# Kernel optimization log

Measured on AMD Instinct MI355X. Metric: run time of the kernel, lower is better.

Reference implementation:

```python
import jax, jax.numpy as jnp
import numpy as np

NEG = -1.0e9

def setup_inputs() -> dict:
    key = jax.random.key(0)
    k1, k2 = jax.random.split(key)
    B, S, D = 4, 4096, 256
    encodings = jax.random.normal(k1, (B, S, D), dtype=jnp.float32)
    # nn.Linear weight [out, in]; Linear applies x @ W.T
    W = jax.random.normal(k2, (D, D), dtype=jnp.float32) * (1.0 / np.sqrt(D))
    return {"encodings": encodings, "W": W}

def reference(encodings, W):
    B, S, D = encodings.shape
    enc_mult_W = jnp.einsum('bsd,ed->bse', encodings, W)          # Linear, no bias
    sims = jnp.einsum('bqd,bkd->bqk', encodings, enc_mult_W)       # E @ (EW^T)^T
    scaled = sims / jnp.asarray(np.sqrt(D), dtype=sims.dtype)
    # causal mask: positions k > q masked out (top-left softmax == 1)
    mask = jnp.triu(jnp.ones((S, S), dtype=bool), k=1)
    scaled = jnp.where(mask[None, :, :], jnp.asarray(NEG, scaled.dtype), scaled)
    attn = jax.nn.softmax(scaled, axis=-1)
    return jnp.einsum('bqk,bkd->bqd', attn, encodings)
```

## Files before the change

### kernel.cpp

```cpp
#include <hip/hip_runtime.h>
#include <hip/hip_bf16.h>
#include <cstdint>
#include <cstddef>

typedef __attribute__((ext_vector_type(4))) float f32x4;
typedef __attribute__((ext_vector_type(8))) short s16x8;
typedef __attribute__((ext_vector_type(4))) unsigned int u32x4;

#define SDIM 4096
#define DDIM 256

#define GLOAD_LDS16(g, s)                                                      \
  __builtin_amdgcn_global_load_lds(                                            \
      (const __attribute__((address_space(1))) void*)(g),                      \
      (__attribute__((address_space(3))) void*)(s), 16, 0, 0)

__device__ __forceinline__ unsigned short cvt_bf16(float f) {
  union { float f; unsigned int u; } v;
  v.f = f;
  unsigned int u = v.u;
  unsigned int r = (u + 0x7FFFu + ((u >> 16) & 1u)) >> 16;
  return (unsigned short)r;
}

__device__ __forceinline__ float bf2f(unsigned short s) {
  union { unsigned int u; float f; } v;
  v.u = ((unsigned int)s) << 16;
  return v.f;
}

__global__ __launch_bounds__(256) void k_prep(const float* __restrict__ E,
                                              const float* __restrict__ W,
                                              unsigned short* __restrict__ Wb,
                                              unsigned short* __restrict__ Vt) {
  __shared__ float tile[64][65];
  const int bid = blockIdx.x;
  const int tid = threadIdx.x;
  if (bid >= 1024) {
    int i = ((bid - 1024) * 256 + tid) * 8;
    f32x4 a = *(const f32x4*)(W + i);
    f32x4 b = *(const f32x4*)(W + i + 4);
    s16x8 o;
#pragma unroll
    for (int j = 0; j < 4; ++j) {
      o[j] = (short)cvt_bf16(a[j]);
      o[4 + j] = (short)cvt_bf16(b[j]);
    }
    *(s16x8*)(Wb + i) = o;
    return;
  }
  const int b = bid >> 8;
  const int d0 = ((bid >> 6) & 3) * 64, s0 = (bid & 63) * 64;
  const int tx = tid & 63, ty = tid >> 6;
#pragma unroll
  for (int i = 0; i < 16; ++i) {
    int sr = i * 4 + ty;
    tile[sr][tx] = E[((size_t)(b * SDIM) + s0 + sr) * DDIM + d0 + tx];
  }
  __syncthreads();
#pragma unroll
  for (int i = 0; i < 16; ++i) {
    int dr = i * 4 + ty;
    Vt[((size_t)(b * DDIM) + d0 + dr) * SDIM + s0 + tx] = cvt_bf16(tile[tx][dr]);
  }
}

__global__ __launch_bounds__(256) void k_proj(const float* __restrict__ E,
                                              const unsigned short* __restrict__ Wb,
                                              unsigned short* __restrict__ Kp) {
  const int tid = threadIdx.x;
  const int w = tid >> 6, l = tid & 63, lhi = l >> 4, llo = l & 15;
  const int m0 = blockIdx.x * 64 + w * 16;
  f32x4 acc[16];
#pragma unroll
  for (int n = 0; n < 16; ++n) acc[n] = (f32x4){0.f, 0.f, 0.f, 0.f};
  const float* arow = E + (size_t)(m0 + llo) * DDIM;
#pragma unroll
  for (int kd = 0; kd < 8; ++kd) {
    const int dbase = kd * 32 + lhi * 8;
    f32x4 a0 = *(const f32x4*)(arow + dbase);
    f32x4 a1 = *(const f32x4*)(arow + dbase + 4);
    s16x8 af;
#pragma unroll
    for (int j = 0; j < 4; ++j) {
      af[j] = (short)cvt_bf16(a0[j]);
      af[4 + j] = (short)cvt_bf16(a1[j]);
    }
#pragma unroll
    for (int n = 0; n < 16; ++n) {
      s16x8 bf = *(const s16x8*)(Wb + (n * 16 + llo) * DDIM + dbase);
      acc[n] = __builtin_amdgcn_mfma_f32_16x16x32_bf16(af, bf, acc[n], 0, 0, 0);
    }
  }
  const float sc = 1.4426950408889634f / 16.0f;
#pragma unroll
  for (int n = 0; n < 16; ++n) {
#pragma unroll
    for (int r = 0; r < 4; ++r) {
      Kp[(size_t)(m0 + lhi * 4 + r) * DDIM + n * 16 + llo] = cvt_bf16(acc[n][r] * sc);
    }
  }
}

__global__ __launch_bounds__(256, 2) void k_attn(const float* __restrict__ E,
                                                 const unsigned short* __restrict__ Kp,
                                                 const unsigned short* __restrict__ Vt,
                                                 unsigned short* __restrict__ Po,
                                                 float* __restrict__ Lp, int nch) {
  __shared__ u32x4 smem4[4736];
  char* smem = (char*)smem4;
  const int tid = threadIdx.x;
  const int l = tid & 63, w = tid >> 6, lhi = l >> 4, llo = l & 15;
  const int u = blockIdx.x % (4 * nch);
  const int p = blockIdx.x / (4 * nch);
  const int b = u & 3, ch = u >> 2;
  const int chb = ch * 4 + b;

  const int trow = tid >> 5;
  const int kcolb = ((tid & 31) << 4) ^ ((trow & 7) << 4);
  const char* KpB = (const char*)Kp + (size_t)b * SDIM * 512;
  const char* VtB = (const char*)Vt + (size_t)b * DDIM * (SDIM * 2);
  const char* vsb = VtB + (size_t)(tid >> 2) * 8192 + (size_t)((tid & 3) * 8) * 2;
  char* sPw = smem + 65536 + w * 2560;

  for (int c2 = 0; c2 < 2; ++c2) {
    const int qt = c2 ? (31 - p) : p;
    const int q0 = qt * 128;
    const int ntile = 4 * (qt + 1);
    if (ntile <= ch) continue;
    const int nst = (ntile - ch + nch - 1) / nch;
    const int wq0 = q0 + w * 32;

    if (c2) __syncthreads();

    s16x8 qf[2][8];
#pragma unroll
    for (int s = 0; s < 2; ++s) {
      const float* Eq = E + ((size_t)(b * SDIM) + wq0 + s * 16 + llo) * DDIM;
#pragma unroll
      for (int kd = 0; kd < 8; ++kd) {
        f32x4 a0 = *(const f32x4*)(Eq + kd * 32 + lhi * 8);
        f32x4 a1 = *(const f32x4*)(Eq + kd * 32 + lhi * 8 + 4);
#pragma unroll
        for (int j = 0; j < 4; ++j) {
          qf[s][kd][j] = (short)cvt_bf16(a0[j]);
          qf[s][kd][4 + j] = (short)cvt_bf16(a1[j]);
        }
      }
    }

    f32x4 oT[2][16];
#pragma unroll
    for (int s = 0; s < 2; ++s)
#pragma unroll
      for (int n = 0; n < 16; ++n) oT[s][n] = (f32x4){0.f, 0.f, 0.f, 0.f};
    float lsum[2] = {0.f, 0.f};

    auto stage = [&](int t) {
      const int kv0 = (ch + nch * t) * 32;
      char* kdst = smem + ((t & 1) * 16384);
      char* vdst = smem + 32768 + ((t & 1) * 16384);
      const char* ks = KpB + (size_t)(kv0 + trow) * 512 + kcolb;
      const char* vs = vsb + (size_t)kv0 * 2;
#pragma unroll
      for (int i = 0; i < 4; ++i)
        GLOAD_LDS16(ks + (size_t)i * 4096, kdst + i * 4096 + tid * 16);
#pragma unroll
      for (int i = 0; i < 4; ++i)
        GLOAD_LDS16(vs + (size_t)i * (64 * 8192), vdst + i * 4096 + tid * 16);
    };

    stage(0);

    for (int t = 0; t < nst; ++t) {
      const int kv0 = (ch + nch * t) * 32;
      const char* kb_ = smem + ((t & 1) * 16384);
      const char* vb_ = smem + 32768 + ((t & 1) * 16384);

      __syncthreads();
      if (t + 1 < nst) stage(t + 1);

#pragma unroll
      for (int kb = 0; kb < 2; ++kb) {
        f32x4 sa0 = (f32x4){0.f, 0.f, 0.f, 0.f};
        f32x4 sa1 = (f32x4){0.f, 0.f, 0.f, 0.f};
        const char* krow = kb_ + (kb * 16 + llo) * 512;
        __builtin_amdgcn_s_setprio(1);
#pragma unroll
        for (int kd = 0; kd < 8; ++kd) {
          s16x8 kf = *(const s16x8*)(krow + ((kd * 64 + lhi * 16) ^ ((llo & 7) << 4)));
          sa0 = __builtin_amdgcn_mfma_f32_16x16x32_bf16(kf, qf[0][kd], sa0, 0, 0, 0);
          sa1 = __builtin_amdgcn_mfma_f32_16x16x32_bf16(kf, qf[1][kd], sa1, 0, 0, 0);
        }
        __builtin_amdgcn_s_setprio(0);
        const int kvr = kv0 + kb * 16 + lhi * 4;
#pragma unroll
        for (int s = 0; s < 2; ++s) {
          const f32x4 sa = s ? sa1 : sa0;
          const int qi = wq0 + s * 16 + llo;
          float pv[4];
#pragma unroll
          for (int rr = 0; rr < 4; ++rr) {
            float v = exp2f(sa[rr] - 32.0f);
            pv[rr] = (kvr + rr > qi) ? 0.0f : v;
          }
          lsum[s] += (pv[0] + pv[1]) + (pv[2] + pv[3]);
          unsigned int w0 = __builtin_amdgcn_perm(__float_as_uint(pv[1]),
                                                  __float_as_uint(pv[0]), 0x07060302u);
          unsigned int w1 = __builtin_amdgcn_perm(__float_as_uint(pv[3]),
                                                  __float_as_uint(pv[2]), 0x07060302u);
          *(uint2*)(sPw + (s * 16 + llo) * 80 + kb * 32 + lhi * 8) = make_uint2(w0, w1);
        }
      }

      s16x8 pb0 = *(const s16x8*)(sPw + llo * 80 + lhi * 16);
      s16x8 pb1 = *(const s16x8*)(sPw + (16 + llo) * 80 + lhi * 16);
      __builtin_amdgcn_s_setprio(1);
#pragma unroll
      for (int n = 0; n < 16; ++n) {
        s16x8 vf = *(const s16x8*)(vb_ + (n * 16 + llo) * 64 + lhi * 16);
        oT[0][n] = __builtin_amdgcn_mfma_f32_16x16x32_bf16(vf, pb0, oT[0][n], 0, 0, 0);
        oT[1][n] = __builtin_amdgcn_mfma_f32_16x16x32_bf16(vf, pb1, oT[1][n], 0, 0, 0);
      }
      __builtin_amdgcn_s_setprio(0);
    }

#pragma unroll
    for (int s = 0; s < 2; ++s) {
      lsum[s] += __shfl_xor(lsum[s], 16);
      lsum[s] += __shfl_xor(lsum[s], 32);
    }
#pragma unroll
    for (int s = 0; s < 2; ++s) {
      const int q = wq0 + s * 16 + llo;
      unsigned short* PoW = Po + ((size_t)chb * SDIM + q) * DDIM;
#pragma unroll
      for (int n = 0; n < 16; ++n) {
        unsigned int w0 = (unsigned int)cvt_bf16(oT[s][n][0]) |
                          ((unsigned int)cvt_bf16(oT[s][n][1]) << 16);
        unsigned int w1 = (unsigned int)cvt_bf16(oT[s][n][2]) |
                          ((unsigned int)cvt_bf16(oT[s][n][3]) << 16);
        *(uint2*)(PoW + n * 16 + lhi * 4) = make_uint2(w0, w1);
      }
      if (lhi == 0) Lp[(size_t)chb * SDIM + q] = lsum[s];
    }
  }
}

__global__ __launch_bounds__(256) void k_merge(const unsigned short* __restrict__ Po,
                                               const float* __restrict__ Lp,
                                               float* __restrict__ out, int nch) {
  const size_t e = ((size_t)blockIdx.x * 256 + threadIdx.x) * 8;
  const size_t f = e >> 8;
  const int s = (int)(f & 4095);
  const int cnt = min(nch, 4 * (s >> 7) + 4);
  float lt = 0.f;
  for (int c = 0; c < cnt; ++c) lt += Lp[(size_t)c * 16384 + f];
  const float inv = 1.0f / lt;
  float acc[8] = {0.f, 0.f, 0.f, 0.f, 0.f, 0.f, 0.f, 0.f};
  for (int c = 0; c < cnt; ++c) {
    s16x8 a = *(const s16x8*)(Po + (size_t)c * 4194304 + e);
#pragma unroll
    for (int j = 0; j < 8; ++j) acc[j] += bf2f((unsigned short)a[j]);
  }
  f32x4 o0, o1;
#pragma unroll
  for (int j = 0; j < 4; ++j) {
    o0[j] = acc[j] * inv;
    o1[j] = acc[4 + j] * inv;
  }
  *(f32x4*)(out + e) = o0;
  *(f32x4*)(out + e + 4) = o1;
}

extern "C" void kernel_launch(void* const* d_in, const int* in_sizes, int n_in,
                              void* d_out, int out_size, void* d_ws, size_t ws_size,
                              hipStream_t stream) {
  (void)in_sizes; (void)n_in; (void)out_size;
  const float* E = (const float*)d_in[0];
  const float* W = (const float*)d_in[1];
  float* out = (float*)d_out;
  char* ws = (char*)d_ws;

  const size_t base = 16777216ull;
  auto need = [&](int c) {
    return base + (size_t)c * 8388608ull + (size_t)c * 65536ull + 262144ull;
  };
  int nch = 2;
  if (ws_size >= need(8)) nch = 8;
  else if (ws_size >= need(4)) nch = 4;

  unsigned short* Kp = (unsigned short*)(ws);
  unsigned short* Vt = (unsigned short*)(ws + 8388608);
  unsigned short* Po = (unsigned short*)(ws + base);
  size_t lp_off = base + (size_t)nch * 8388608ull;
  float* Lp = (float*)(ws + lp_off);
  unsigned short* Wb = (unsigned short*)(ws + lp_off + (size_t)nch * 65536ull);

  k_prep<<<dim3(1056), dim3(256), 0, stream>>>(E, W, Wb, Vt);
  k_proj<<<dim3(256), dim3(256), 0, stream>>>(E, Wb, Kp);
  k_attn<<<dim3(16 * 4 * nch), dim3(256), 0, stream>>>(E, Kp, Vt, Po, Lp, nch);
  k_merge<<<dim3(2048), dim3(256), 0, stream>>>(Po, Lp, out, nch);
}
```

Before: 128.5 us.

## Fuse V transpose into projection, split paired q-tiles into separate blocks, nontemporal stores

The V transpose-and-convert moves out of the prep kernel and into the projection kernel, reusing the bf16 E tile already staged in LDS, so E is read once fewer. The attention kernel no longer pairs q-tile p with 31-p inside one block. Each block now handles a single q-tile, with twice as many blocks launched and the heaviest tiles scheduled first. This gives up the built-in load balancing of pairing in exchange for finer-grained scheduling. Partial outputs and the Lp sums use nontemporal stores and loads to reduce cache pollution.

```diff
diff --git a/kernel.cpp b/kernel.cpp
--- a/kernel.cpp
+++ b/kernel.cpp
@@ -29,48 +29,29 @@
   return v.f;
 }
 
-__global__ __launch_bounds__(256) void k_prep(const float* __restrict__ E,
-                                              const float* __restrict__ W,
-                                              unsigned short* __restrict__ Wb,
-                                              unsigned short* __restrict__ Vt) {
-  __shared__ float tile[64][65];
-  const int bid = blockIdx.x;
-  const int tid = threadIdx.x;
-  if (bid >= 1024) {
-    int i = ((bid - 1024) * 256 + tid) * 8;
-    f32x4 a = *(const f32x4*)(W + i);
-    f32x4 b = *(const f32x4*)(W + i + 4);
-    s16x8 o;
-#pragma unroll
-    for (int j = 0; j < 4; ++j) {
-      o[j] = (short)cvt_bf16(a[j]);
-      o[4 + j] = (short)cvt_bf16(b[j]);
-    }
-    *(s16x8*)(Wb + i) = o;
-    return;
-  }
-  const int b = bid >> 8;
-  const int d0 = ((bid >> 6) & 3) * 64, s0 = (bid & 63) * 64;
-  const int tx = tid & 63, ty = tid >> 6;
-#pragma unroll
-  for (int i = 0; i < 16; ++i) {
-    int sr = i * 4 + ty;
-    tile[sr][tx] = E[((size_t)(b * SDIM) + s0 + sr) * DDIM + d0 + tx];
-  }
-  __syncthreads();
-#pragma unroll
-  for (int i = 0; i < 16; ++i) {
-    int dr = i * 4 + ty;
-    Vt[((size_t)(b * DDIM) + d0 + dr) * SDIM + s0 + tx] = cvt_bf16(tile[tx][dr]);
-  }
-}
-
-__global__ __launch_bounds__(256) void k_proj(const float* __restrict__ E,
-                                              const unsigned short* __restrict__ Wb,
-                                              unsigned short* __restrict__ Kp) {
+__global__ __launch_bounds__(256) void k_convw(const float* __restrict__ W,
+                                               unsigned short* __restrict__ Wb) {
+  int i = (blockIdx.x * 256 + threadIdx.x) * 8;
+  f32x4 a = *(const f32x4*)(W + i);
+  f32x4 b = *(const f32x4*)(W + i + 4);
+  s16x8 o;
+#pragma unroll
+  for (int j = 0; j < 4; ++j) {
+    o[j] = (short)cvt_bf16(a[j]);
+    o[4 + j] = (short)cvt_bf16(b[j]);
+  }
+  *(s16x8*)(Wb + i) = o;
+}
+
+__global__ __launch_bounds__(256) void k_projv(const float* __restrict__ E,
+                                               const unsigned short* __restrict__ Wb,
+                                               unsigned short* __restrict__ Kp,
+                                               unsigned short* __restrict__ Vt) {
+  __shared__ unsigned short tile[64][264];
   const int tid = threadIdx.x;
   const int w = tid >> 6, l = tid & 63, lhi = l >> 4, llo = l & 15;
-  const int m0 = blockIdx.x * 64 + w * 16;
+  const int m0g = blockIdx.x * 64;
+  const int m0 = m0g + w * 16;
   f32x4 acc[16];
 #pragma unroll
   for (int n = 0; n < 16; ++n) acc[n] = (f32x4){0.f, 0.f, 0.f, 0.f};
@@ -86,10 +67,24 @@
       af[j] = (short)cvt_bf16(a0[j]);
       af[4 + j] = (short)cvt_bf16(a1[j]);
     }
+    *(s16x8*)(&tile[w * 16 + llo][dbase]) = af;
 #pragma unroll
     for (int n = 0; n < 16; ++n) {
       s16x8 bf = *(const s16x8*)(Wb + (n * 16 + llo) * DDIM + dbase);
       acc[n] = __builtin_amdgcn_mfma_f32_16x16x32_bf16(af, bf, acc[n], 0, 0, 0);
+    }
+  }
+  __syncthreads();
+  {
+    const int d = tid;
+    const int b = m0g >> 12, s0 = m0g & 4095;
+    unsigned short* vo = Vt + ((size_t)(b * DDIM) + d) * SDIM + s0;
+#pragma unroll
+    for (int g = 0; g < 8; ++g) {
+      s16x8 pk;
+#pragma unroll
+      for (int j = 0; j < 8; ++j) pk[j] = (short)tile[g * 8 + j][d];
+      *(s16x8*)(vo + g * 8) = pk;
     }
   }
   const float sc = 1.4426950408889634f / 16.0f;
@@ -112,138 +107,135 @@
   const int tid = threadIdx.x;
   const int l = tid & 63, w = tid >> 6, lhi = l >> 4, llo = l & 15;
   const int u = blockIdx.x % (4 * nch);
-  const int p = blockIdx.x / (4 * nch);
+  const int t_ = blockIdx.x / (4 * nch);
+  const int qt = 31 - t_;
   const int b = u & 3, ch = u >> 2;
+  const int q0 = qt * 128;
   const int chb = ch * 4 + b;
+  const int ntile = 4 * (qt + 1);
+  if (ntile <= ch) return;
+  const int nst = (ntile - ch + nch - 1) / nch;
+  const int wq0 = q0 + w * 32;
+
+  s16x8 qf[2][8];
+#pragma unroll
+  for (int s = 0; s < 2; ++s) {
+    const float* Eq = E + ((size_t)(b * SDIM) + wq0 + s * 16 + llo) * DDIM;
+#pragma unroll
+    for (int kd = 0; kd < 8; ++kd) {
+      f32x4 a0 = *(const f32x4*)(Eq + kd * 32 + lhi * 8);
+      f32x4 a1 = *(const f32x4*)(Eq + kd * 32 + lhi * 8 + 4);
+#pragma unroll
+      for (int j = 0; j < 4; ++j) {
+        qf[s][kd][j] = (short)cvt_bf16(a0[j]);
+        qf[s][kd][4 + j] = (short)cvt_bf16(a1[j]);
+      }
+    }
+  }
+
+  f32x4 oT[2][16];
+#pragma unroll
+  for (int s = 0; s < 2; ++s)
+#pragma unroll
+    for (int n = 0; n < 16; ++n) oT[s][n] = (f32x4){0.f, 0.f, 0.f, 0.f};
+  float lsum[2] = {0.f, 0.f};
 
   const int trow = tid >> 5;
   const int kcolb = ((tid & 31) << 4) ^ ((trow & 7) << 4);
   const char* KpB = (const char*)Kp + (size_t)b * SDIM * 512;
   const char* VtB = (const char*)Vt + (size_t)b * DDIM * (SDIM * 2);
   const char* vsb = VtB + (size_t)(tid >> 2) * 8192 + (size_t)((tid & 3) * 8) * 2;
+
+  auto stage = [&](int t) {
+    const int kv0 = (ch + nch * t) * 32;
+    char* kdst = smem + ((t & 1) * 16384);
+    char* vdst = smem + 32768 + ((t & 1) * 16384);
+    const char* ks = KpB + (size_t)(kv0 + trow) * 512 + kcolb;
+    const char* vs = vsb + (size_t)kv0 * 2;
+#pragma unroll
+    for (int i = 0; i < 4; ++i)
+      GLOAD_LDS16(ks + (size_t)i * 4096, kdst + i * 4096 + tid * 16);
+#pragma unroll
+    for (int i = 0; i < 4; ++i)
+      GLOAD_LDS16(vs + (size_t)i * (64 * 8192), vdst + i * 4096 + tid * 16);
+  };
+
+  stage(0);
   char* sPw = smem + 65536 + w * 2560;
 
-  for (int c2 = 0; c2 < 2; ++c2) {
-    const int qt = c2 ? (31 - p) : p;
-    const int q0 = qt * 128;
-    const int ntile = 4 * (qt + 1);
-    if (ntile <= ch) continue;
-    const int nst = (ntile - ch + nch - 1) / nch;
-    const int wq0 = q0 + w * 32;
-
-    if (c2) __syncthreads();
-
-    s16x8 qf[2][8];
-#pragma unroll
-    for (int s = 0; s < 2; ++s) {
-      const float* Eq = E + ((size_t)(b * SDIM) + wq0 + s * 16 + llo) * DDIM;
+  for (int t = 0; t < nst; ++t) {
+    const int kv0 = (ch + nch * t) * 32;
+    const char* kb_ = smem + ((t & 1) * 16384);
+    const char* vb_ = smem + 32768 + ((t & 1) * 16384);
+
+    __syncthreads();
+    if (t + 1 < nst) stage(t + 1);
+
+#pragma unroll
+    for (int kb = 0; kb < 2; ++kb) {
+      f32x4 sa0 = (f32x4){0.f, 0.f, 0.f, 0.f};
+      f32x4 sa1 = (f32x4){0.f, 0.f, 0.f, 0.f};
+      const char* krow = kb_ + (kb * 16 + llo) * 512;
+      __builtin_amdgcn_s_setprio(1);
 #pragma unroll
       for (int kd = 0; kd < 8; ++kd) {
-        f32x4 a0 = *(const f32x4*)(Eq + kd * 32 + lhi * 8);
-        f32x4 a1 = *(const f32x4*)(Eq + kd * 32 + lhi * 8 + 4);
-#pragma unroll
-        for (int j = 0; j < 4; ++j) {
-          qf[s][kd][j] = (short)cvt_bf16(a0[j]);
-          qf[s][kd][4 + j] = (short)cvt_bf16(a1[j]);
-        }
-      }
-    }
-
-    f32x4 oT[2][16];
-#pragma unroll
-    for (int s = 0; s < 2; ++s)
-#pragma unroll
-      for (int n = 0; n < 16; ++n) oT[s][n] = (f32x4){0.f, 0.f, 0.f, 0.f};
-    float lsum[2] = {0.f, 0.f};
-
-    auto stage = [&](int t) {
-      const int kv0 = (ch + nch * t) * 32;
-      char* kdst = smem + ((t & 1) * 16384);
-      char* vdst = smem + 32768 + ((t & 1) * 16384);
-      const char* ks = KpB + (size_t)(kv0 + trow) * 512 + kcolb;
-      const char* vs = vsb + (size_t)kv0 * 2;
-#pragma unroll
-      for (int i = 0; i < 4; ++i)
-        GLOAD_LDS16(ks + (size_t)i * 4096, kdst + i * 4096 + tid * 16);
-#pragma unroll
-      for (int i = 0; i < 4; ++i)
-        GLOAD_LDS16(vs + (size_t)i * (64 * 8192), vdst + i * 4096 + tid * 16);
-    };
-
-    stage(0);
-
-    for (int t = 0; t < nst; ++t) {
-      const int kv0 = (ch + nch * t) * 32;
-      const char* kb_ = smem + ((t & 1) * 16384);
-      const char* vb_ = smem + 32768 + ((t & 1) * 16384);
-
-      __syncthreads();
-      if (t + 1 < nst) stage(t + 1);
-
-#pragma unroll
-      for (int kb = 0; kb < 2; ++kb) {
-        f32x4 sa0 = (f32x4){0.f, 0.f, 0.f, 0.f};
-        f32x4 sa1 = (f32x4){0.f, 0.f, 0.f, 0.f};
-        const char* krow = kb_ + (kb * 16 + llo) * 512;
-        __builtin_amdgcn_s_setprio(1);
-#pragma unroll
-        for (int kd = 0; kd < 8; ++kd) {
-          s16x8 kf = *(const s16x8*)(krow + ((kd * 64 + lhi * 16) ^ ((llo & 7) << 4)));
-          sa0 = __builtin_amdgcn_mfma_f32_16x16x32_bf16(kf, qf[0][kd], sa0, 0, 0, 0);
-          sa1 = __builtin_amdgcn_mfma_f32_16x16x32_bf16(kf, qf[1][kd], sa1, 0, 0, 0);
-        }
-        __builtin_amdgcn_s_setprio(0);
-        const int kvr = kv0 + kb * 16 + lhi * 4;
-#pragma unroll
-        for (int s = 0; s < 2; ++s) {
-          const f32x4 sa = s ? sa1 : sa0;
-          const int qi = wq0 + s * 16 + llo;
-          float pv[4];
-#pragma unroll
-          for (int rr = 0; rr < 4; ++rr) {
-            float v = exp2f(sa[rr] - 32.0f);
-            pv[rr] = (kvr + rr > qi) ? 0.0f : v;
-          }
-          lsum[s] += (pv[0] + pv[1]) + (pv[2] + pv[3]);
-          unsigned int w0 = __builtin_amdgcn_perm(__float_as_uint(pv[1]),
-                                                  __float_as_uint(pv[0]), 0x07060302u);
-          unsigned int w1 = __builtin_amdgcn_perm(__float_as_uint(pv[3]),
-                                                  __float_as_uint(pv[2]), 0x07060302u);
-          *(uint2*)(sPw + (s * 16 + llo) * 80 + kb * 32 + lhi * 8) = make_uint2(w0, w1);
-        }
-      }
-
-      s16x8 pb0 = *(const s16x8*)(sPw + llo * 80 + lhi * 16);
-      s16x8 pb1 = *(const s16x8*)(sPw + (16 + llo) * 80 + lhi * 16);
-      __builtin_amdgcn_s_setprio(1);
-#pragma unroll
-      for (int n = 0; n < 16; ++n) {
-        s16x8 vf = *(const s16x8*)(vb_ + (n * 16 + llo) * 64 + lhi * 16);
-        oT[0][n] = __builtin_amdgcn_mfma_f32_16x16x32_bf16(vf, pb0, oT[0][n], 0, 0, 0);
-        oT[1][n] = __builtin_amdgcn_mfma_f32_16x16x32_bf16(vf, pb1, oT[1][n], 0, 0, 0);
+        s16x8 kf = *(const s16x8*)(krow + ((kd * 64 + lhi * 16) ^ ((llo & 7) << 4)));
+        sa0 = __builtin_amdgcn_mfma_f32_16x16x32_bf16(kf, qf[0][kd], sa0, 0, 0, 0);
+        sa1 = __builtin_amdgcn_mfma_f32_16x16x32_bf16(kf, qf[1][kd], sa1, 0, 0, 0);
       }
       __builtin_amdgcn_s_setprio(0);
-    }
-
-#pragma unroll
-    for (int s = 0; s < 2; ++s) {
-      lsum[s] += __shfl_xor(lsum[s], 16);
-      lsum[s] += __shfl_xor(lsum[s], 32);
-    }
-#pragma unroll
-    for (int s = 0; s < 2; ++s) {
-      const int q = wq0 + s * 16 + llo;
-      unsigned short* PoW = Po + ((size_t)chb * SDIM + q) * DDIM;
-#pragma unroll
-      for (int n = 0; n < 16; ++n) {
-        unsigned int w0 = (unsigned int)cvt_bf16(oT[s][n][0]) |
-                          ((unsigned int)cvt_bf16(oT[s][n][1]) << 16);
-        unsigned int w1 = (unsigned int)cvt_bf16(oT[s][n][2]) |
-                          ((unsigned int)cvt_bf16(oT[s][n][3]) << 16);
-        *(uint2*)(PoW + n * 16 + lhi * 4) = make_uint2(w0, w1);
+      const int kvr = kv0 + kb * 16 + lhi * 4;
+#pragma unroll
+      for (int s = 0; s < 2; ++s) {
+        const f32x4 sa = s ? sa1 : sa0;
+        const int qi = wq0 + s * 16 + llo;
+        float pv[4];
+#pragma unroll
+        for (int rr = 0; rr < 4; ++rr) {
+          float v = exp2f(sa[rr] - 32.0f);
+          pv[rr] = (kvr + rr > qi) ? 0.0f : v;
+        }
+        lsum[s] += (pv[0] + pv[1]) + (pv[2] + pv[3]);
+        unsigned int w0 = __builtin_amdgcn_perm(__float_as_uint(pv[1]),
+                                                __float_as_uint(pv[0]), 0x07060302u);
+        unsigned int w1 = __builtin_amdgcn_perm(__float_as_uint(pv[3]),
+                                                __float_as_uint(pv[2]), 0x07060302u);
+        *(uint2*)(sPw + (s * 16 + llo) * 80 + kb * 32 + lhi * 8) = make_uint2(w0, w1);
       }
-      if (lhi == 0) Lp[(size_t)chb * SDIM + q] = lsum[s];
-    }
+    }
+
+    s16x8 pb0 = *(const s16x8*)(sPw + llo * 80 + lhi * 16);
+    s16x8 pb1 = *(const s16x8*)(sPw + (16 + llo) * 80 + lhi * 16);
+    __builtin_amdgcn_s_setprio(1);
+#pragma unroll
+    for (int n = 0; n < 16; ++n) {
+      s16x8 vf = *(const s16x8*)(vb_ + (n * 16 + llo) * 64 + lhi * 16);
+      oT[0][n] = __builtin_amdgcn_mfma_f32_16x16x32_bf16(vf, pb0, oT[0][n], 0, 0, 0);
+      oT[1][n] = __builtin_amdgcn_mfma_f32_16x16x32_bf16(vf, pb1, oT[1][n], 0, 0, 0);
+    }
+    __builtin_amdgcn_s_setprio(0);
+  }
+
+#pragma unroll
+  for (int s = 0; s < 2; ++s) {
+    lsum[s] += __shfl_xor(lsum[s], 16);
+    lsum[s] += __shfl_xor(lsum[s], 32);
+  }
+#pragma unroll
+  for (int s = 0; s < 2; ++s) {
+    const int q = wq0 + s * 16 + llo;
+    unsigned short* PoW = Po + ((size_t)chb * SDIM + q) * DDIM;
+#pragma unroll
+    for (int n = 0; n < 16; ++n) {
+      unsigned int w0 = (unsigned int)cvt_bf16(oT[s][n][0]) |
+                        ((unsigned int)cvt_bf16(oT[s][n][1]) << 16);
+      unsigned int w1 = (unsigned int)cvt_bf16(oT[s][n][2]) |
+                        ((unsigned int)cvt_bf16(oT[s][n][3]) << 16);
+      unsigned long long v64 = (unsigned long long)w0 | ((unsigned long long)w1 << 32);
+      __builtin_nontemporal_store(v64, (unsigned long long*)(PoW + n * 16 + lhi * 4));
+    }
+    if (lhi == 0)
+      __builtin_nontemporal_store(lsum[s], &Lp[(size_t)chb * SDIM + q]);
   }
 }
 
@@ -255,11 +247,12 @@
   const int s = (int)(f & 4095);
   const int cnt = min(nch, 4 * (s >> 7) + 4);
   float lt = 0.f;
-  for (int c = 0; c < cnt; ++c) lt += Lp[(size_t)c * 16384 + f];
+  for (int c = 0; c < cnt; ++c)
+    lt += __builtin_nontemporal_load(&Lp[(size_t)c * 16384 + f]);
   const float inv = 1.0f / lt;
   float acc[8] = {0.f, 0.f, 0.f, 0.f, 0.f, 0.f, 0.f, 0.f};
   for (int c = 0; c < cnt; ++c) {
-    s16x8 a = *(const s16x8*)(Po + (size_t)c * 4194304 + e);
+    s16x8 a = __builtin_nontemporal_load((const s16x8*)(Po + (size_t)c * 4194304 + e));
 #pragma unroll
     for (int j = 0; j < 8; ++j) acc[j] += bf2f((unsigned short)a[j]);
   }
@@ -297,8 +290,8 @@
   float* Lp = (float*)(ws + lp_off);
   unsigned short* Wb = (unsigned short*)(ws + lp_off + (size_t)nch * 65536ull);
 
-  k_prep<<<dim3(1056), dim3(256), 0, stream>>>(E, W, Wb, Vt);
-  k_proj<<<dim3(256), dim3(256), 0, stream>>>(E, Wb, Kp);
-  k_attn<<<dim3(16 * 4 * nch), dim3(256), 0, stream>>>(E, Kp, Vt, Po, Lp, nch);
+  k_convw<<<dim3(32), dim3(256), 0, stream>>>(W, Wb);
+  k_projv<<<dim3(256), dim3(256), 0, stream>>>(E, Wb, Kp, Vt);
+  k_attn<<<dim3(32 * 4 * nch), dim3(256), 0, stream>>>(E, Kp, Vt, Po, Lp, nch);
   k_merge<<<dim3(2048), dim3(256), 0, stream>>>(Po, Lp, out, nch);
 }
```

After: 151.9 us. 18.3% more time.
